# Optimization experiments

Measured on AMD Instinct MI355X. Metric: run time of the kernel, lower is better.

Reference implementation:

```python
import jax, jax.numpy as jnp
import numpy as np

K = 10          # negatives per anchor (init k)
GAMMA = 1.0     # margin (init gamma)
CHUNK = 32      # anchor chunk for L1 cdist to bound [chunk, N, d] intermediate


def _l1_cdist(a, b):
    """Cityblock distances. a: [A, d], b: [N, d] -> [A, N], chunked over A."""
    A, d = a.shape
    a_c = a.reshape(A // CHUNK, CHUNK, d)
    def f(ac):  # ac: [CHUNK, d] -> [CHUNK, N]
        return jnp.sum(jnp.abs(ac[:, None, :] - b[None, :, :]), axis=-1)
    return jax.lax.map(f, a_c).reshape(A, b.shape[0])


def setup_inputs() -> dict:
    key = jax.random.key(0)
    k1, k2, k3, k4 = jax.random.split(key, 4)
    N, D, A = 20000, 128, 1024
    return {
        "out1": jax.random.normal(k1, (N, D), dtype=jnp.float32),
        "out2": jax.random.normal(k2, (N, D), dtype=jnp.float32),
        "anchor1": jax.random.randint(k3, (A,), 0, N),
        "anchor2": jax.random.randint(k4, (A,), 0, N),
    }


def reference(out1, out2, anchor1, anchor2):
    a1 = out1[anchor1]              # [A, D]
    a2 = out2[anchor2]              # [A, D]
    # neg sampling: k nearest (smallest L1 distance) rows of the other side
    d1 = _l1_cdist(a1, out2)        # [A, N]
    d2 = _l1_cdist(a2, out1)        # [A, N]
    neg1 = jnp.argsort(d1, axis=1)[:, :K]   # [A, K] indices into out2
    neg2 = jnp.argsort(d2, axis=1)[:, :K]   # [A, K] indices into out1
    neg_e1 = out2[neg1]             # [A, K, D]
    neg_e2 = out1[neg2]             # [A, K, D]
    A_pos = jnp.sum(jnp.abs(a1 - a2), axis=1)   # [A] positive L1 distance
    Dm = A_pos + GAMMA                           # [A]
    B1 = -jnp.sum(jnp.abs(a1[:, None, :] - neg_e1), axis=2)  # [A, K]
    L1 = jnp.sum(jax.nn.relu(Dm[:, None] + B1))
    B2 = -jnp.sum(jnp.abs(a2[:, None, :] - neg_e2), axis=2)  # [A, K]
    L2 = jnp.sum(jax.nn.relu(Dm[:, None] + B2))
    return (L1 + L2) / (anchor1.shape[0] * K)
```

## Files before the change

### kernel.cpp

```cpp
#include <hip/hip_runtime.h>

#define N_PTS 20000
#define DIMS  128
#define A_CNT 1024
#define KNEG  10
#define NTILES 157
#define NCHUNK (NTILES * 16)
#define NCHUNK_REAL 2500
#define BIGV  1e18f
#define BIGI  0x7F000000
#define CAND_CAP 768
#define PT_CAP   768
#define AB_BLOCKS 1024
#define QR_BLOCKS 625
#define RPART     1250

__device__ __forceinline__ unsigned int sad_u8(unsigned int a, unsigned int b, unsigned int c) {
#if __has_builtin(__builtin_amdgcn_sad_u8)
    return __builtin_amdgcn_sad_u8(a, b, c);
#else
    unsigned int d;
    asm("v_sad_u8 %0, %1, %2, %3" : "=v"(d) : "v"(a), "v"(b), "v"(c));
    return d;
#endif
}

__global__ void absmax_kernel(const float* __restrict__ a, const float* __restrict__ b,
                              float* __restrict__ wsAmax, float* __restrict__ outZero) {
    __shared__ float sm[4];
    const int n4 = N_PTS * DIMS / 4;
    const int stride = gridDim.x * blockDim.x;
    float m = 0.f;
    for (int i = blockIdx.x * blockDim.x + threadIdx.x; i < 2 * n4; i += stride) {
        const float4 v = (i < n4) ? ((const float4*)a)[i] : ((const float4*)b)[i - n4];
        m = fmaxf(m, fmaxf(fmaxf(fabsf(v.x), fabsf(v.y)), fmaxf(fabsf(v.z), fabsf(v.w))));
    }
#pragma unroll
    for (int s = 1; s < 64; s <<= 1) m = fmaxf(m, __shfl_xor(m, s, 64));
    if ((threadIdx.x & 63) == 0) sm[threadIdx.x >> 6] = m;
    __syncthreads();
    if (threadIdx.x == 0) {
        wsAmax[blockIdx.x] = fmaxf(fmaxf(sm[0], sm[1]), fmaxf(sm[2], sm[3]));
        if (blockIdx.x == 0) *outZero = 0.f;
    }
}

__global__ void quantR_kernel(const float* __restrict__ o1, const float* __restrict__ o2,
                              unsigned int* __restrict__ q1, unsigned int* __restrict__ q2,
                              float* __restrict__ Ra, float* __restrict__ Rb,
                              const float* __restrict__ wsAmax,
                              float* __restrict__ wsRmaxPart) {
    __shared__ float sm[4];
    __shared__ float sM;
    const int tid = threadIdx.x;
    {
        const float4 v = ((const float4*)wsAmax)[tid];
        float m = fmaxf(fmaxf(v.x, v.y), fmaxf(v.z, v.w));
#pragma unroll
        for (int s = 1; s < 64; s <<= 1) m = fmaxf(m, __shfl_xor(m, s, 64));
        if ((tid & 63) == 0) sm[tid >> 6] = m;
        __syncthreads();
        if (tid == 0) sM = fmaxf(fmaxf(sm[0], sm[1]), fmaxf(sm[2], sm[3]));
        __syncthreads();
    }
    const float M = sM;
    const float s = 127.0f / M;

    const int side = blockIdx.y;
    const float* src = side ? o2 : o1;
    unsigned int* dst = side ? q2 : q1;
    float* Rrow = side ? Rb : Ra;
    const int g = blockIdx.x * 256 + tid;
    const int row = g >> 3;
    const int sub = g & 7;
    const float4* s4 = (const float4*)(src + (size_t)row * DIMS + sub * 16);
    unsigned int* d = dst + (size_t)row * 32 + sub * 4;
    float rs = 0.f;
#pragma unroll
    for (int m = 0; m < 4; ++m) {
        const float4 v = s4[m];
        const float f0 = v.x * s + 127.0f, f1 = v.y * s + 127.0f;
        const float f2 = v.z * s + 127.0f, f3 = v.w * s + 127.0f;
        const float q0 = rintf(f0), q1v = rintf(f1), q2v = rintf(f2), q3 = rintf(f3);
        rs += fabsf(q0 - f0) + fabsf(q1v - f1) + fabsf(q2v - f2) + fabsf(q3 - f3);
        d[m] = (unsigned int)q0 | ((unsigned int)q1v << 8) |
               ((unsigned int)q2v << 16) | ((unsigned int)q3 << 24);
    }
    rs += __shfl_xor(rs, 1, 64);
    rs += __shfl_xor(rs, 2, 64);
    rs += __shfl_xor(rs, 4, 64);
    const float R = rs + 1.0f;
    if (sub == 0) Rrow[row] = R;
    float rm = R;
    rm = fmaxf(rm, __shfl_xor(rm, 8, 64));
    rm = fmaxf(rm, __shfl_xor(rm, 16, 64));
    rm = fmaxf(rm, __shfl_xor(rm, 32, 64));
    if ((tid & 63) == 0) sm[tid >> 6] = rm;
    __syncthreads();
    if (tid == 0)
        wsRmaxPart[blockIdx.y * QR_BLOCKS + blockIdx.x] =
            fmaxf(fmaxf(sm[0], sm[1]), fmaxf(sm[2], sm[3]));
}

__global__ __launch_bounds__(256, 4)
void dist_sad_kernel(const unsigned int* __restrict__ q1, const unsigned int* __restrict__ q2,
                     const int* __restrict__ anchor1, const int* __restrict__ anchor2,
                     unsigned short* __restrict__ minOut,
                     const float* __restrict__ wsRmaxPart, float* __restrict__ rmaxOut) {
    __shared__ unsigned int sA[64 * 32];
    __shared__ unsigned int sP[128 * 32];

    const int tile = blockIdx.x;
    const int ag   = blockIdx.y;
    const int side = blockIdx.z;

    if (tile == 0 && ag == 0 && side == 0 && threadIdx.x < 64) {
        float r = 0.f;
        for (int i = threadIdx.x; i < RPART; i += 64) r = fmaxf(r, wsRmaxPart[i]);
#pragma unroll
        for (int s = 1; s < 64; s <<= 1) r = fmaxf(r, __shfl_xor(r, s, 64));
        if (threadIdx.x == 0) *rmaxOut = r;
    }

    const unsigned int* aData = side ? q2 : q1;
    const unsigned int* pData = side ? q1 : q2;
    const int*          aIdx  = side ? anchor2 : anchor1;

    const int tid = threadIdx.x;
    const int tx = tid & 15;
    const int ty = tid >> 4;

    {
        const int ra = tid >> 2;
        const int qa = tid & 3;
        const unsigned int* aRow = aData + (size_t)aIdx[ag * 64 + ra] * 32;
        const uint4 v0 = *(const uint4*)(aRow + qa * 4);
        const uint4 v1 = *(const uint4*)(aRow + (qa + 4) * 4);
        const int rot = ra >> 3;
        *(uint4*)&sA[ra * 32 + (((qa + rot) & 7) << 2)]     = v0;
        *(uint4*)&sA[ra * 32 + (((qa + 4 + rot) & 7) << 2)] = v1;
    }
    {
        const int rp = tid >> 1;
        const int h  = tid & 1;
        const int prow = tile * 128 + rp;
        const bool pvalid = prow < N_PTS;
        const uint4* pRow4 = (const uint4*)(pData + (size_t)prow * 32 + h * 16);
        const int rot = rp >> 3;
#pragma unroll
        for (int j = 0; j < 4; ++j) {
            const uint4 v = pvalid ? pRow4[j]
                                   : make_uint4(0xFFFFFFFFu, 0xFFFFFFFFu, 0xFFFFFFFFu, 0xFFFFFFFFu);
            const int blk = h * 4 + j;
            *(uint4*)&sP[rp * 32 + (((blk + rot) & 7) << 2)] = v;
        }
    }
    __syncthreads();

    unsigned int acc[4][8];
#pragma unroll
    for (int i = 0; i < 4; ++i)
#pragma unroll
        for (int j = 0; j < 8; ++j) acc[i][j] = 0u;

    const int ty4 = ty * 4;
    const int tx8 = tx * 8;

#pragma unroll 2
    for (int bk = 0; bk < 8; ++bk) {
        uint4 A[4], P[8];
        const int aslot = ((bk + (ty >> 1)) & 7) << 2;
        const int pslot = ((bk + tx) & 7) << 2;
#pragma unroll
        for (int i = 0; i < 4; ++i) A[i] = *(const uint4*)&sA[(ty4 + i) * 32 + aslot];
#pragma unroll
        for (int j = 0; j < 8; ++j) P[j] = *(const uint4*)&sP[(tx8 + j) * 32 + pslot];
#pragma unroll
        for (int i = 0; i < 4; ++i)
#pragma unroll
            for (int j = 0; j < 8; ++j) {
                unsigned int s = sad_u8(A[i].x, P[j].x, acc[i][j]);
                s = sad_u8(A[i].y, P[j].y, s);
                s = sad_u8(A[i].z, P[j].z, s);
                acc[i][j] = sad_u8(A[i].w, P[j].w, s);
            }
    }

    const size_t outBase = (size_t)side * A_CNT * NCHUNK;
#pragma unroll
    for (int i = 0; i < 4; ++i) {
        unsigned int m = min(min(min(acc[i][0], acc[i][1]), min(acc[i][2], acc[i][3])),
                             min(min(acc[i][4], acc[i][5]), min(acc[i][6], acc[i][7])));
        minOut[outBase + (size_t)(ag * 64 + ty4 + i) * NCHUNK + tile * 16 + tx] =
            (unsigned short)m;
    }
}

__global__ __launch_bounds__(256, 4)
void select_kernel(const float* __restrict__ out1, const float* __restrict__ out2,
                   const unsigned int* __restrict__ q1, const unsigned int* __restrict__ q2,
                   const int* __restrict__ anchor1, const int* __restrict__ anchor2,
                   const unsigned short* __restrict__ minIn,
                   const float* __restrict__ R1, const float* __restrict__ R2,
                   const float* __restrict__ rmaxIn, float* __restrict__ out) {
    const int bid = blockIdx.x;
    const int side = bid >> 10;
    const int ai = bid & 1023;
    const int tid = threadIdx.x;
    const int lane = tid & 63;
    const int wv = tid >> 6;

    const float* aDataF = side ? out2 : out1;
    const float* pDataF = side ? out1 : out2;
    const unsigned int* aDataQ = side ? q2 : q1;
    const unsigned int* pDataQ = side ? q1 : q2;
    const float* Ranc = side ? R2 : R1;
    const int* aIdx = side ? anchor2 : anchor1;

    __shared__ int candCount, pointCount;
    __shared__ int candList[CAND_CAP];
    __shared__ int ptList[PT_CAP];
    __shared__ __align__(16) float sDist[PT_CAP];
    __shared__ int sMin[4];
    __shared__ int sCnt[4];
    __shared__ float wSum[4];
    __shared__ float sDm;

    const int arow = aIdx[ai];
    const uint4 qa4 = ((const uint4*)(aDataQ + (size_t)arow * 32))[lane & 7];
    if (tid == 0) { candCount = 0; pointCount = 0; }

    if (wv == 0) {
        const int r1 = anchor1[ai], r2 = anchor2[ai];
        const float2 x1 = ((const float2*)(out1 + (size_t)r1 * DIMS))[lane];
        const float2 x2 = ((const float2*)(out2 + (size_t)r2 * DIMS))[lane];
        float dm = fabsf(x1.x - x2.x) + fabsf(x1.y - x2.y);
#pragma unroll
        for (int s = 1; s < 64; s <<= 1) dm += __shfl_xor(dm, s, 64);
        if (lane == 0) sDm = dm + 1.0f;
    }

    const unsigned short* mbase = minIn + ((size_t)side * A_CNT + ai) * NCHUNK;
    int mv[10];
#pragma unroll
    for (int j = 0; j < 10; ++j) {
        const int c = tid + 256 * j;
        mv[j] = (c < NCHUNK_REAL) ? (int)mbase[c] : BIGI;
    }
    int lmin = BIGI;
#pragma unroll
    for (int j = 0; j < 10; ++j) lmin = min(lmin, mv[j]);
#pragma unroll
    for (int s = 1; s < 64; s <<= 1) lmin = min(lmin, __shfl_xor(lmin, s, 64));
    if (lane == 0) sMin[wv] = lmin;
    __syncthreads();
    const int m1 = min(min(sMin[0], sMin[1]), min(sMin[2], sMin[3]));

    int E = m1 + 192;
    for (;;) {
        int c = 0;
#pragma unroll
        for (int j = 0; j < 10; ++j) c += (mv[j] <= E) ? 1 : 0;
#pragma unroll
        for (int s = 1; s < 64; s <<= 1) c += __shfl_xor(c, s, 64);
        if (lane == 0) sCnt[wv] = c;
        __syncthreads();
        const int total = sCnt[0] + sCnt[1] + sCnt[2] + sCnt[3];
        __syncthreads();
        if (total >= KNEG) break;
        E += 192;
    }
    int lo = (E == m1 + 192) ? (m1 - 1) : (E - 192);
    int hi = E;
#pragma unroll
    for (int it = 0; it < 3; ++it) {
        const int mid = (lo + hi) >> 1;
        int c = 0;
#pragma unroll
        for (int j = 0; j < 10; ++j) c += (mv[j] <= mid) ? 1 : 0;
#pragma unroll
        for (int s = 1; s < 64; s <<= 1) c += __shfl_xor(c, s, 64);
        if (lane == 0) sCnt[wv] = c;
        __syncthreads();
        const int total = sCnt[0] + sCnt[1] + sCnt[2] + sCnt[3];
        __syncthreads();
        if (total >= KNEG) hi = mid; else lo = mid;
    }
    const float Rmax = *rmaxIn;
    const float thr = (float)hi + 2.0f * Ranc[arow] + 2.0f * Rmax + 4.0f;

#pragma unroll
    for (int j = 0; j < 10; ++j) {
        const int c = tid + 256 * j;
        if (c < NCHUNK_REAL && (float)mv[j] <= thr) {
            const int pos = atomicAdd(&candCount, 1);
            if (pos < CAND_CAP) candList[pos] = c;
        }
    }
    __syncthreads();
    const int cc = min(candCount, CAND_CAP);

    const int psub = lane >> 3;
    const int seg  = lane & 7;
    for (int s0 = wv * 4; s0 < cc; s0 += 16) {
        uint4 qp[4];
        int ptv[4];
#pragma unroll
        for (int u = 0; u < 4; ++u) {
            const int s = s0 + u;
            const int c = candList[(s < cc) ? s : s0];
            ptv[u] = c * 8 + psub;
            qp[u] = ((const uint4*)(pDataQ + (size_t)ptv[u] * 32))[seg];
        }
#pragma unroll
        for (int u = 0; u < 4; ++u) {
            unsigned int d = sad_u8(qa4.x, qp[u].x, 0u);
            d = sad_u8(qa4.y, qp[u].y, d);
            d = sad_u8(qa4.z, qp[u].z, d);
            d = sad_u8(qa4.w, qp[u].w, d);
            int di = (int)d;
            di += __shfl_xor(di, 1, 64);
            di += __shfl_xor(di, 2, 64);
            di += __shfl_xor(di, 4, 64);
            if ((s0 + u) < cc && seg == 0 && (float)di <= thr) {
                const int pos = atomicAdd(&pointCount, 1);
                if (pos < PT_CAP) ptList[pos] = ptv[u];
            }
        }
    }
    __syncthreads();
    const int pc = min(pointCount, PT_CAP);

    const int pt4 = tid >> 2;
    const int qq  = tid & 3;
    float4 av[8];
    {
        const float4* aF4 = (const float4*)(aDataF + (size_t)arow * DIMS) + qq * 8;
#pragma unroll
        for (int q = 0; q < 8; ++q) av[q] = aF4[q];
    }
    for (int base = 0; base < pc; base += 64) {
        const int idx = base + pt4;
        float s01 = 0.f, s23 = 0.f;
        if (idx < pc) {
            const int pt = ptList[idx];
            const float4* p4 = (const float4*)(pDataF + (size_t)pt * DIMS) + qq * 8;
#pragma unroll
            for (int q = 0; q < 8; ++q) {
                const float4 pv = p4[q];
                s01 += fabsf(av[q].x - pv.x) + fabsf(av[q].y - pv.y);
                s23 += fabsf(av[q].z - pv.z) + fabsf(av[q].w - pv.w);
            }
        }
        float s = s01 + s23;
        s += __shfl_xor(s, 1, 64);
        s += __shfl_xor(s, 2, 64);
        if (qq == 0 && idx < pc) sDist[idx] = s;
    }
    __syncthreads();

    const float dm = sDm;
    float contrib = 0.f;
    if (pc <= 256) {
        const int i0 = tid;
        const float v0 = (i0 < pc) ? sDist[i0] : BIGV;
        int r0 = 0;
        int j = 0;
        for (; j + 2 <= pc; j += 2) {
            const float2 vj = *(const float2*)&sDist[j];
            r0 += ((vj.x < v0) || (vj.x == v0 && j < i0)) ? 1 : 0;
            r0 += ((vj.y < v0) || (vj.y == v0 && (j + 1) < i0)) ? 1 : 0;
        }
        if (j < pc) {
            const float vj = sDist[j];
            r0 += ((vj < v0) || (vj == v0 && j < i0)) ? 1 : 0;
        }
        if (i0 < pc && r0 < KNEG) contrib = fmaxf(dm - v0, 0.f);
    } else {
        const int i0 = tid, i1 = tid + 256, i2 = tid + 512;
        float v0 = BIGV, v1 = BIGV, v2 = BIGV;
        if (i0 < pc) v0 = sDist[i0];
        if (i1 < pc) v1 = sDist[i1];
        if (i2 < pc) v2 = sDist[i2];
        int r0 = 0, r1 = 0, r2 = 0;
        for (int j = 0; j < pc; ++j) {
            const float vj = sDist[j];
            r0 += (vj < v0) || (vj == v0 && j < i0);
            r1 += (vj < v1) || (vj == v1 && j < i1);
            r2 += (vj < v2) || (vj == v2 && j < i2);
        }
        if (i0 < pc && r0 < KNEG) contrib += fmaxf(dm - v0, 0.f);
        if (i1 < pc && r1 < KNEG) contrib += fmaxf(dm - v1, 0.f);
        if (i2 < pc && r2 < KNEG) contrib += fmaxf(dm - v2, 0.f);
    }
#pragma unroll
    for (int s = 1; s < 64; s <<= 1) contrib += __shfl_xor(contrib, s, 64);
    if (lane == 0) wSum[wv] = contrib;
    __syncthreads();
    if (tid == 0)
        atomicAdd(out, (wSum[0] + wSum[1] + wSum[2] + wSum[3]) * (1.0f / (A_CNT * KNEG)));
}

extern "C" void kernel_launch(void* const* d_in, const int* in_sizes, int n_in,
                              void* d_out, int out_size, void* d_ws, size_t ws_size,
                              hipStream_t stream) {
    const float* out1    = (const float*)d_in[0];
    const float* out2    = (const float*)d_in[1];
    const int*   anchor1 = (const int*)d_in[2];
    const int*   anchor2 = (const int*)d_in[3];
    float* out = (float*)d_out;

    unsigned int* q1 = (unsigned int*)d_ws;
    unsigned int* q2 = q1 + (size_t)N_PTS * DIMS / 4;
    unsigned short* minbuf = (unsigned short*)(q2 + (size_t)N_PTS * DIMS / 4);
    float* R1 = (float*)(minbuf + (size_t)2 * A_CNT * NCHUNK);
    float* R2 = R1 + N_PTS;
    float* wsAmax = R2 + N_PTS;
    float* wsRmaxPart = wsAmax + AB_BLOCKS;
    float* rmax = wsRmaxPart + 1280;

    hipLaunchKernelGGL(absmax_kernel, dim3(AB_BLOCKS), dim3(256), 0, stream,
                       out1, out2, wsAmax, out);
    hipLaunchKernelGGL(quantR_kernel, dim3(QR_BLOCKS, 2), dim3(256), 0, stream,
                       out1, out2, q1, q2, R1, R2, wsAmax, wsRmaxPart);

    dim3 gridA(NTILES, 16, 2);
    hipLaunchKernelGGL(dist_sad_kernel, gridA, dim3(256), 0, stream,
                       q1, q2, anchor1, anchor2, minbuf, wsRmaxPart, rmax);
    hipLaunchKernelGGL(select_kernel, dim3(2048), dim3(256), 0, stream,
                       out1, out2, q1, q2, anchor1, anchor2, minbuf, R1, R2, rmax, out);
}
```

Before: 206.0 us.

## Split select kernel per anchor into two halves and merge top-k in new kernel

```diff
diff --git a/kernel.cpp b/kernel.cpp
--- a/kernel.cpp
+++ b/kernel.cpp
@@ -6,7 +6,8 @@
 #define KNEG  10
 #define NTILES 157
 #define NCHUNK (NTILES * 16)
-#define NCHUNK_REAL 2500
+#define NPAIR  (NCHUNK / 2)
+#define NPAIR_REAL 1250
 #define BIGV  1e18f
 #define BIGI  0x7F000000
 #define CAND_CAP 768
@@ -202,10 +203,11 @@
                    const int* __restrict__ anchor1, const int* __restrict__ anchor2,
                    const unsigned short* __restrict__ minIn,
                    const float* __restrict__ R1, const float* __restrict__ R2,
-                   const float* __restrict__ rmaxIn, float* __restrict__ out) {
+                   const float* __restrict__ rmaxIn, float* __restrict__ wsTop) {
     const int bid = blockIdx.x;
-    const int side = bid >> 10;
-    const int ai = bid & 1023;
+    const int side = bid >> 11;
+    const int ai = (bid >> 1) & 1023;
+    const int h  = bid & 1;
     const int tid = threadIdx.x;
     const int lane = tid & 63;
     const int wv = tid >> 6;
@@ -223,29 +225,25 @@
     __shared__ __align__(16) float sDist[PT_CAP];
     __shared__ int sMin[4];
     __shared__ int sCnt[4];
-    __shared__ float wSum[4];
-    __shared__ float sDm;
 
     const int arow = aIdx[ai];
     const uint4 qa4 = ((const uint4*)(aDataQ + (size_t)arow * 32))[lane & 7];
     if (tid == 0) { candCount = 0; pointCount = 0; }
 
-    if (wv == 0) {
-        const int r1 = anchor1[ai], r2 = anchor2[ai];
-        const float2 x1 = ((const float2*)(out1 + (size_t)r1 * DIMS))[lane];
-        const float2 x2 = ((const float2*)(out2 + (size_t)r2 * DIMS))[lane];
-        float dm = fabsf(x1.x - x2.x) + fabsf(x1.y - x2.y);
-#pragma unroll
-        for (int s = 1; s < 64; s <<= 1) dm += __shfl_xor(dm, s, 64);
-        if (lane == 0) sDm = dm + 1.0f;
-    }
-
-    const unsigned short* mbase = minIn + ((size_t)side * A_CNT + ai) * NCHUNK;
+    const unsigned int* mbase =
+        (const unsigned int*)minIn + ((size_t)side * A_CNT + ai) * NPAIR;
     int mv[10];
 #pragma unroll
-    for (int j = 0; j < 10; ++j) {
-        const int c = tid + 256 * j;
-        mv[j] = (c < NCHUNK_REAL) ? (int)mbase[c] : BIGI;
+    for (int u = 0; u < 5; ++u) {
+        const int p = tid + 256 * u;
+        if (p < NPAIR_REAL) {
+            const unsigned int v = mbase[p];
+            mv[2 * u]     = (int)(v & 0xFFFFu);
+            mv[2 * u + 1] = (int)(v >> 16);
+        } else {
+            mv[2 * u] = BIGI;
+            mv[2 * u + 1] = BIGI;
+        }
     }
     int lmin = BIGI;
 #pragma unroll
@@ -290,11 +288,11 @@
     const float thr = (float)hi + 2.0f * Ranc[arow] + 2.0f * Rmax + 4.0f;
 
 #pragma unroll
-    for (int j = 0; j < 10; ++j) {
-        const int c = tid + 256 * j;
-        if (c < NCHUNK_REAL && (float)mv[j] <= thr) {
+    for (int u = 0; u < 5; ++u) {
+        const int p = tid + 256 * u;
+        if (p < NPAIR_REAL && (float)mv[2 * u + h] <= thr) {
             const int pos = atomicAdd(&candCount, 1);
-            if (pos < CAND_CAP) candList[pos] = c;
+            if (pos < CAND_CAP) candList[pos] = 2 * p + h;
         }
     }
     __syncthreads();
@@ -359,8 +357,8 @@
     }
     __syncthreads();
 
-    const float dm = sDm;
-    float contrib = 0.f;
+    float* top = wsTop + (((size_t)side * A_CNT + ai) * 2 + h) * 10;
+    if (tid >= pc && tid < KNEG) top[tid] = BIGV;
     if (pc <= 256) {
         const int i0 = tid;
         const float v0 = (i0 < pc) ? sDist[i0] : BIGV;
@@ -375,7 +373,7 @@
             const float vj = sDist[j];
             r0 += ((vj < v0) || (vj == v0 && j < i0)) ? 1 : 0;
         }
-        if (i0 < pc && r0 < KNEG) contrib = fmaxf(dm - v0, 0.f);
+        if (i0 < pc && r0 < KNEG) top[r0] = v0;
     } else {
         const int i0 = tid, i1 = tid + 256, i2 = tid + 512;
         float v0 = BIGV, v1 = BIGV, v2 = BIGV;
@@ -389,10 +387,40 @@
             r1 += (vj < v1) || (vj == v1 && j < i1);
             r2 += (vj < v2) || (vj == v2 && j < i2);
         }
-        if (i0 < pc && r0 < KNEG) contrib += fmaxf(dm - v0, 0.f);
-        if (i1 < pc && r1 < KNEG) contrib += fmaxf(dm - v1, 0.f);
-        if (i2 < pc && r2 < KNEG) contrib += fmaxf(dm - v2, 0.f);
-    }
+        if (i0 < pc && r0 < KNEG) top[r0] = v0;
+        if (i1 < pc && r1 < KNEG) top[r1] = v1;
+        if (i2 < pc && r2 < KNEG) top[r2] = v2;
+    }
+}
+
+__global__ __launch_bounds__(256, 4)
+void merge_kernel(const float* __restrict__ out1, const float* __restrict__ out2,
+                  const int* __restrict__ anchor1, const int* __restrict__ anchor2,
+                  const float* __restrict__ wsTop, float* __restrict__ out) {
+    __shared__ float wSum[4];
+    const int tid = threadIdx.x;
+    const int lane = tid & 63;
+    const int wv = tid >> 6;
+    const int t = blockIdx.x * 4 + wv;
+    const int ai = t & 1023;
+
+    float v = (lane < 20) ? wsTop[(size_t)t * 20 + lane] : BIGV;
+    int rank = 0;
+#pragma unroll
+    for (int j = 0; j < 20; ++j) {
+        const float vj = __shfl(v, j, 64);
+        rank += ((vj < v) || (vj == v && j < lane)) ? 1 : 0;
+    }
+
+    const int r1 = anchor1[ai], r2 = anchor2[ai];
+    const float2 x1 = ((const float2*)(out1 + (size_t)r1 * DIMS))[lane];
+    const float2 x2 = ((const float2*)(out2 + (size_t)r2 * DIMS))[lane];
+    float dm = fabsf(x1.x - x2.x) + fabsf(x1.y - x2.y);
+#pragma unroll
+    for (int s = 1; s < 64; s <<= 1) dm += __shfl_xor(dm, s, 64);
+    dm += 1.0f;
+
+    float contrib = (lane < 20 && rank < KNEG) ? fmaxf(dm - v, 0.f) : 0.f;
 #pragma unroll
     for (int s = 1; s < 64; s <<= 1) contrib += __shfl_xor(contrib, s, 64);
     if (lane == 0) wSum[wv] = contrib;
@@ -418,6 +446,7 @@
     float* wsAmax = R2 + N_PTS;
     float* wsRmaxPart = wsAmax + AB_BLOCKS;
     float* rmax = wsRmaxPart + 1280;
+    float* wsTop = rmax + 4;
 
     hipLaunchKernelGGL(absmax_kernel, dim3(AB_BLOCKS), dim3(256), 0, stream,
                        out1, out2, wsAmax, out);
@@ -427,6 +456,8 @@
     dim3 gridA(NTILES, 16, 2);
     hipLaunchKernelGGL(dist_sad_kernel, gridA, dim3(256), 0, stream,
                        q1, q2, anchor1, anchor2, minbuf, wsRmaxPart, rmax);
-    hipLaunchKernelGGL(select_kernel, dim3(2048), dim3(256), 0, stream,
-                       out1, out2, q1, q2, anchor1, anchor2, minbuf, R1, R2, rmax, out);
-}
+    hipLaunchKernelGGL(select_kernel, dim3(4096), dim3(256), 0, stream,
+                       out1, out2, q1, q2, anchor1, anchor2, minbuf, R1, R2, rmax, wsTop);
+    hipLaunchKernelGGL(merge_kernel, dim3(512), dim3(256), 0, stream,
+                       out1, out2, anchor1, anchor2, wsTop, out);
+}
```

Result: no change. 209.8 us (+1.8%).

## Add per-tile super-minimum level to prune chunk scans in selection

Applied to the files above, without the earlier changes.

```diff
diff --git a/kernel.cpp b/kernel.cpp
--- a/kernel.cpp
+++ b/kernel.cpp
@@ -7,9 +7,10 @@
 #define NTILES 157
 #define NCHUNK (NTILES * 16)
 #define NCHUNK_REAL 2500
+#define SUPER_PITCH 160
 #define BIGV  1e18f
 #define BIGI  0x7F000000
-#define CAND_CAP 768
+#define CAND_CAP 1024
 #define PT_CAP   768
 #define AB_BLOCKS 1024
 #define QR_BLOCKS 625
@@ -105,7 +106,7 @@
 __global__ __launch_bounds__(256, 4)
 void dist_sad_kernel(const unsigned int* __restrict__ q1, const unsigned int* __restrict__ q2,
                      const int* __restrict__ anchor1, const int* __restrict__ anchor2,
-                     unsigned short* __restrict__ minOut,
+                     unsigned short* __restrict__ minOut, unsigned short* __restrict__ superOut,
                      const float* __restrict__ wsRmaxPart, float* __restrict__ rmaxOut) {
     __shared__ unsigned int sA[64 * 32];
     __shared__ unsigned int sP[128 * 32];
@@ -193,6 +194,14 @@
                              min(min(acc[i][4], acc[i][5]), min(acc[i][6], acc[i][7])));
         minOut[outBase + (size_t)(ag * 64 + ty4 + i) * NCHUNK + tile * 16 + tx] =
             (unsigned short)m;
+        unsigned int sm = m;
+        sm = min(sm, __shfl_xor(sm, 1, 64));
+        sm = min(sm, __shfl_xor(sm, 2, 64));
+        sm = min(sm, __shfl_xor(sm, 4, 64));
+        sm = min(sm, __shfl_xor(sm, 8, 64));
+        if (tx == 0)
+            superOut[((size_t)side * A_CNT + ag * 64 + ty4 + i) * SUPER_PITCH + tile] =
+                (unsigned short)sm;
     }
 }
 
@@ -201,6 +210,7 @@
                    const unsigned int* __restrict__ q1, const unsigned int* __restrict__ q2,
                    const int* __restrict__ anchor1, const int* __restrict__ anchor2,
                    const unsigned short* __restrict__ minIn,
+                   const unsigned short* __restrict__ superIn,
                    const float* __restrict__ R1, const float* __restrict__ R2,
                    const float* __restrict__ rmaxIn, float* __restrict__ out) {
     const int bid = blockIdx.x;
@@ -217,7 +227,8 @@
     const float* Ranc = side ? R2 : R1;
     const int* aIdx = side ? anchor2 : anchor1;
 
-    __shared__ int candCount, pointCount;
+    __shared__ int candCount, pointCount, tileCount;
+    __shared__ int tileList[160];
     __shared__ int candList[CAND_CAP];
     __shared__ int ptList[PT_CAP];
     __shared__ __align__(16) float sDist[PT_CAP];
@@ -228,7 +239,7 @@
 
     const int arow = aIdx[ai];
     const uint4 qa4 = ((const uint4*)(aDataQ + (size_t)arow * 32))[lane & 7];
-    if (tid == 0) { candCount = 0; pointCount = 0; }
+    if (tid == 0) { candCount = 0; pointCount = 0; tileCount = 0; }
 
     if (wv == 0) {
         const int r1 = anchor1[ai], r2 = anchor2[ai];
@@ -240,16 +251,14 @@
         if (lane == 0) sDm = dm + 1.0f;
     }
 
-    const unsigned short* mbase = minIn + ((size_t)side * A_CNT + ai) * NCHUNK;
-    int mv[10];
-#pragma unroll
-    for (int j = 0; j < 10; ++j) {
-        const int c = tid + 256 * j;
-        mv[j] = (c < NCHUNK_REAL) ? (int)mbase[c] : BIGI;
-    }
-    int lmin = BIGI;
-#pragma unroll
-    for (int j = 0; j < 10; ++j) lmin = min(lmin, mv[j]);
+    const unsigned short* sbase = superIn + ((size_t)side * A_CNT + ai) * SUPER_PITCH;
+    int v0 = BIGI, v1 = BIGI;
+    if (tid < SUPER_PITCH / 2) {
+        const unsigned int v = ((const unsigned int*)sbase)[tid];
+        if (2 * tid < NTILES)     v0 = (int)(v & 0xFFFFu);
+        if (2 * tid + 1 < NTILES) v1 = (int)(v >> 16);
+    }
+    int lmin = min(v0, v1);
 #pragma unroll
     for (int s = 1; s < 64; s <<= 1) lmin = min(lmin, __shfl_xor(lmin, s, 64));
     if (lane == 0) sMin[wv] = lmin;
@@ -258,9 +267,7 @@
 
     int E = m1 + 192;
     for (;;) {
-        int c = 0;
-#pragma unroll
-        for (int j = 0; j < 10; ++j) c += (mv[j] <= E) ? 1 : 0;
+        int c = ((v0 <= E) ? 1 : 0) + ((v1 <= E) ? 1 : 0);
 #pragma unroll
         for (int s = 1; s < 64; s <<= 1) c += __shfl_xor(c, s, 64);
         if (lane == 0) sCnt[wv] = c;
@@ -275,9 +282,7 @@
 #pragma unroll
     for (int it = 0; it < 3; ++it) {
         const int mid = (lo + hi) >> 1;
-        int c = 0;
-#pragma unroll
-        for (int j = 0; j < 10; ++j) c += (mv[j] <= mid) ? 1 : 0;
+        int c = ((v0 <= mid) ? 1 : 0) + ((v1 <= mid) ? 1 : 0);
 #pragma unroll
         for (int s = 1; s < 64; s <<= 1) c += __shfl_xor(c, s, 64);
         if (lane == 0) sCnt[wv] = c;
@@ -289,10 +294,23 @@
     const float Rmax = *rmaxIn;
     const float thr = (float)hi + 2.0f * Ranc[arow] + 2.0f * Rmax + 4.0f;
 
-#pragma unroll
-    for (int j = 0; j < 10; ++j) {
-        const int c = tid + 256 * j;
-        if (c < NCHUNK_REAL && (float)mv[j] <= thr) {
+    if (tid < SUPER_PITCH / 2) {
+        if ((float)v0 <= thr) {
+            const int pos = atomicAdd(&tileCount, 1);
+            tileList[pos] = 2 * tid;
+        }
+        if ((float)v1 <= thr) {
+            const int pos = atomicAdd(&tileCount, 1);
+            tileList[pos] = 2 * tid + 1;
+        }
+    }
+    __syncthreads();
+    const int tc = tileCount;
+
+    const unsigned short* mbase = minIn + ((size_t)side * A_CNT + ai) * NCHUNK;
+    for (int i = tid >> 4; i < tc; i += 16) {
+        const int c = tileList[i] * 16 + (tid & 15);
+        if (c < NCHUNK_REAL && (float)mbase[c] <= thr) {
             const int pos = atomicAdd(&candCount, 1);
             if (pos < CAND_CAP) candList[pos] = c;
         }
@@ -363,35 +381,35 @@
     float contrib = 0.f;
     if (pc <= 256) {
         const int i0 = tid;
-        const float v0 = (i0 < pc) ? sDist[i0] : BIGV;
+        const float v = (i0 < pc) ? sDist[i0] : BIGV;
         int r0 = 0;
         int j = 0;
         for (; j + 2 <= pc; j += 2) {
             const float2 vj = *(const float2*)&sDist[j];
-            r0 += ((vj.x < v0) || (vj.x == v0 && j < i0)) ? 1 : 0;
-            r0 += ((vj.y < v0) || (vj.y == v0 && (j + 1) < i0)) ? 1 : 0;
+            r0 += ((vj.x < v) || (vj.x == v && j < i0)) ? 1 : 0;
+            r0 += ((vj.y < v) || (vj.y == v && (j + 1) < i0)) ? 1 : 0;
         }
         if (j < pc) {
             const float vj = sDist[j];
-            r0 += ((vj < v0) || (vj == v0 && j < i0)) ? 1 : 0;
-        }
-        if (i0 < pc && r0 < KNEG) contrib = fmaxf(dm - v0, 0.f);
+            r0 += ((vj < v) || (vj == v && j < i0)) ? 1 : 0;
+        }
+        if (i0 < pc && r0 < KNEG) contrib = fmaxf(dm - v, 0.f);
     } else {
         const int i0 = tid, i1 = tid + 256, i2 = tid + 512;
-        float v0 = BIGV, v1 = BIGV, v2 = BIGV;
-        if (i0 < pc) v0 = sDist[i0];
-        if (i1 < pc) v1 = sDist[i1];
-        if (i2 < pc) v2 = sDist[i2];
+        float va = BIGV, vb = BIGV, vc = BIGV;
+        if (i0 < pc) va = sDist[i0];
+        if (i1 < pc) vb = sDist[i1];
+        if (i2 < pc) vc = sDist[i2];
         int r0 = 0, r1 = 0, r2 = 0;
         for (int j = 0; j < pc; ++j) {
             const float vj = sDist[j];
-            r0 += (vj < v0) || (vj == v0 && j < i0);
-            r1 += (vj < v1) || (vj == v1 && j < i1);
-            r2 += (vj < v2) || (vj == v2 && j < i2);
-        }
-        if (i0 < pc && r0 < KNEG) contrib += fmaxf(dm - v0, 0.f);
-        if (i1 < pc && r1 < KNEG) contrib += fmaxf(dm - v1, 0.f);
-        if (i2 < pc && r2 < KNEG) contrib += fmaxf(dm - v2, 0.f);
+            r0 += (vj < va) || (vj == va && j < i0);
+            r1 += (vj < vb) || (vj == vb && j < i1);
+            r2 += (vj < vc) || (vj == vc && j < i2);
+        }
+        if (i0 < pc && r0 < KNEG) contrib += fmaxf(dm - va, 0.f);
+        if (i1 < pc && r1 < KNEG) contrib += fmaxf(dm - vb, 0.f);
+        if (i2 < pc && r2 < KNEG) contrib += fmaxf(dm - vc, 0.f);
     }
 #pragma unroll
     for (int s = 1; s < 64; s <<= 1) contrib += __shfl_xor(contrib, s, 64);
@@ -413,7 +431,8 @@
     unsigned int* q1 = (unsigned int*)d_ws;
     unsigned int* q2 = q1 + (size_t)N_PTS * DIMS / 4;
     unsigned short* minbuf = (unsigned short*)(q2 + (size_t)N_PTS * DIMS / 4);
-    float* R1 = (float*)(minbuf + (size_t)2 * A_CNT * NCHUNK);
+    unsigned short* superbuf = minbuf + (size_t)2 * A_CNT * NCHUNK;
+    float* R1 = (float*)(superbuf + (size_t)2 * A_CNT * SUPER_PITCH);
     float* R2 = R1 + N_PTS;
     float* wsAmax = R2 + N_PTS;
     float* wsRmaxPart = wsAmax + AB_BLOCKS;
@@ -426,7 +445,8 @@
 
     dim3 gridA(NTILES, 16, 2);
     hipLaunchKernelGGL(dist_sad_kernel, gridA, dim3(256), 0, stream,
-                       q1, q2, anchor1, anchor2, minbuf, wsRmaxPart, rmax);
+                       q1, q2, anchor1, anchor2, minbuf, superbuf, wsRmaxPart, rmax);
     hipLaunchKernelGGL(select_kernel, dim3(2048), dim3(256), 0, stream,
-                       out1, out2, q1, q2, anchor1, anchor2, minbuf, R1, R2, rmax, out);
-}
+                       out1, out2, q1, q2, anchor1, anchor2, minbuf, superbuf,
+                       R1, R2, rmax, out);
+}
```

Measured after the change: 218.7 us. +6.1%, slower.
